# Optimization experiments

Hardware: AMD Instinct MI355X
Metric: run time of the kernel (lower is better)

The kernel has to match this reference:

```python
import jax, jax.numpy as jnp
import numpy as np

RNN = 64

def linear(x, W, b):
    return x @ W.T + b

def sample_logprob(key, logits):
    # Categorical(softmax(logits)): sample + log_prob of the sample
    s = jax.random.categorical(key, logits)
    lp = jnp.take_along_axis(jax.nn.log_softmax(logits, -1), s[:, None], 1)[:, 0]
    return s, lp

def lstm_encode(inst, embed, W_ih, W_hh, b_ih, b_hh):
    # torch.nn.LSTMCell unrolled over the sequence; gate order i,f,g,o
    x = embed[inst]                              # [B,S,64]
    B = inst.shape[0]
    def step(carry, xt):
        h, c = carry
        gates = xt @ W_ih.T + b_ih + h @ W_hh.T + b_hh   # [B,256]
        i, f, g, o = jnp.split(gates, 4, axis=-1)
        c = jax.nn.sigmoid(f) * c + jax.nn.sigmoid(i) * jnp.tanh(g)
        h = jax.nn.sigmoid(o) * jnp.tanh(c)
        return (h, c), None
    h0 = jnp.zeros((B, RNN), x.dtype)
    (h, _), _ = jax.lax.scan(step, (h0, h0), jnp.swapaxes(x, 0, 1))
    return h

def setup_inputs():
    key = jax.random.key(0)
    ks = jax.random.split(key, 20)
    B, S, V = 16384, 32, 1000
    def nrm(k, shape, scale=0.05):
        return jax.random.normal(k, shape, jnp.float32) * scale
    return {
        "inst0": jax.random.randint(ks[0], (B, S), 0, V + 1),
        "inst1": jax.random.randint(ks[1], (B, S), 0, V + 1),
        "canvas0": jax.random.randint(ks[2], (B, 25, 4), 0, 5).astype(jnp.int32),
        "canvas1": jax.random.randint(ks[3], (B, 25, 4), 0, 5).astype(jnp.int32),
        "ref": jax.random.randint(ks[4], (B, 4), 0, 5).astype(jnp.int32),
        "embed": nrm(ks[5], (V + 1, RNN)),
        "W_ih": nrm(ks[6], (4 * RNN, RNN)), "W_hh": nrm(ks[7], (4 * RNN, RNN)),
        "b_ih": jnp.zeros(4 * RNN), "b_hh": jnp.zeros(4 * RNN),
        "Wc": nrm(ks[8], (3, RNN)), "bc": jnp.zeros(3),
        "Ws": nrm(ks[9], (3, RNN)), "bs": jnp.zeros(3),
        "Wl": nrm(ks[10], (25, RNN)), "bl": jnp.zeros(25),
        "Wr1": nrm(ks[11], (32, RNN + 4)), "br1": jnp.zeros(32),
        "Wr2": nrm(ks[12], (1, 32)), "br2": jnp.zeros(1),
        "Wp": nrm(ks[13], (8, RNN)), "bp": jnp.zeros(8),
    }

def reference(inst0, inst1, canvas0, canvas1, ref, embed, W_ih, W_hh, b_ih, b_hh,
              Wc, bc, Ws, bs, Wl, bl, Wr1, br1, Wr2, br2, Wp, bp):
    B = inst0.shape[0]
    kk = jax.random.split(jax.random.key(42), 7)
    final_canvas = canvas1                                   # [B,25,4]

    def step_rewards(loc_predict, color_sample, shape_sample):
        valid = (loc_predict >= 0) & (loc_predict < 25)
        pt = jnp.take_along_axis(final_canvas,
                                 jnp.clip(loc_predict, 0, 24)[:, None, None],
                                 axis=1)[:, 0]               # [B,4]
        ok = valid & (pt.sum(-1) >= 0)
        loc_r = jnp.where(ok, 1.0, -1.0)
        col_r = jnp.where(ok, jnp.where(color_sample == pt[:, 0], 1.0, -1.0), 0.0)
        shp_r = jnp.where(ok, jnp.where(shape_sample == pt[:, 1], 1.0, -1.0), 0.0)
        return loc_r, col_r, shp_r

    # ---- dialog step 0: absolute location ----
    h0 = lstm_encode(inst0, embed, W_ih, W_hh, b_ih, b_hh)
    cs0, clp0 = sample_logprob(kk[0], linear(h0, Wc, bc))
    ss0, slp0 = sample_logprob(kk[1], linear(h0, Ws, bs))
    loc0, llp0 = sample_logprob(kk[2], linear(h0, Wl, bl))
    loc_r0, col_r0, _ = step_rewards(loc0, cs0, ss0)

    # ---- dialog step 1: relative location w.r.t. attended ref object ----
    h1 = lstm_encode(inst1, embed, W_ih, W_hh, b_ih, b_hh)
    cs1, clp1 = sample_logprob(kk[3], linear(h1, Wc, bc))
    ss1, slp1 = sample_logprob(kk[4], linear(h1, Ws, bs))
    ls1, llp1 = sample_logprob(kk[5], linear(h1, Wp, bp))    # 8-way offset
    prev = canvas0.astype(h1.dtype)                          # [B,25,4]
    feat = jnp.concatenate([jnp.broadcast_to(h1[:, None, :], (B, 25, RNN)), prev], 2)  # [B,25,68]
    att_logits = (jax.nn.relu(feat @ Wr1.T + br1) @ Wr2.T + br2)[:, :, 0]              # [B,25]
    att_sample, alp1 = sample_logprob(kk[6], att_logits)
    ref_obj = jnp.take_along_axis(canvas0, att_sample[:, None, None], axis=1)[:, 0]    # [B,4]
    att_reward = ((ref_obj == ref).sum(-1) == 4).astype(jnp.float32) * 2.0 - 1.0
    offsets = jnp.array([[-1, 0], [1, 0], [0, 1], [0, -1],
                         [-1, -1], [-1, 1], [1, -1], [1, 1]], jnp.int32)
    off = offsets[ls1]
    loc1 = (ref_obj[:, 2] + off[:, 0]) * 5 + (ref_obj[:, 3] + off[:, 1])
    loc_r1, col_r1, _ = step_rewards(loc1, cs1, ss1)

    logp = jnp.stack([clp0, slp0, llp0, clp1, slp1, llp1, alp1])          # [7,B]
    # NB: original appends step_loc_reward into shape_rewards (kept verbatim)
    rew = jnp.stack([loc_r0, col_r0, loc_r0, loc_r1, col_r1, loc_r1, att_reward])  # [7,B]
    return logp, rew
```

## Files before the change

kernel.cpp:

```cpp
#include <hip/hip_runtime.h>
#include <hip/hip_bf16.h>
#include <stdint.h>
#include <math.h>

#define NB 16384
#define NSEQ 32
#define NV 1001
#define NROWS 32768

#define CHK 272
#define RTG (8 * CHK)
#define SPL (2 * RTG)
#define HBUF (3 * SPL)

typedef __attribute__((ext_vector_type(8))) short bf16x8;
typedef __attribute__((ext_vector_type(4))) float f32x4;

__device__ __forceinline__ void tf2x32(uint32_t k0, uint32_t k1,
                                       uint32_t x0, uint32_t x1,
                                       uint32_t& o0, uint32_t& o1) {
  const uint32_t ks0 = k0, ks1 = k1, ks2 = k0 ^ k1 ^ 0x1BD11BDAu;
  x0 += ks0; x1 += ks1;
  const int rA[4] = {13, 15, 26, 6};
  const int rB[4] = {17, 29, 16, 24};
#pragma unroll
  for (int i = 0; i < 4; ++i) { x0 += x1; x1 = (x1 << rA[i]) | (x1 >> (32 - rA[i])); x1 ^= x0; }
  x0 += ks1; x1 += ks2 + 1u;
#pragma unroll
  for (int i = 0; i < 4; ++i) { x0 += x1; x1 = (x1 << rB[i]) | (x1 >> (32 - rB[i])); x1 ^= x0; }
  x0 += ks2; x1 += ks0 + 2u;
#pragma unroll
  for (int i = 0; i < 4; ++i) { x0 += x1; x1 = (x1 << rA[i]) | (x1 >> (32 - rA[i])); x1 ^= x0; }
  x0 += ks0; x1 += ks1 + 3u;
#pragma unroll
  for (int i = 0; i < 4; ++i) { x0 += x1; x1 = (x1 << rB[i]) | (x1 >> (32 - rB[i])); x1 ^= x0; }
  x0 += ks1; x1 += ks2 + 4u;
#pragma unroll
  for (int i = 0; i < 4; ++i) { x0 += x1; x1 = (x1 << rA[i]) | (x1 >> (32 - rA[i])); x1 ^= x0; }
  o0 = x0 + ks2; o1 = x1 + ks0 + 5u;
}

__device__ __forceinline__ float gumbel_from_bits(uint32_t bits) {
  uint32_t fb = (bits >> 9) | 0x3f800000u;
  float u = __uint_as_float(fb) - 1.0f;
  u = fmaxf(u, 1.17549435e-38f);
  return -logf(-logf(u));
}

__device__ __forceinline__ float sigm(float x) { return 1.0f / (1.0f + __expf(-x)); }
__device__ __forceinline__ float tanh_(float x) {
  float e = __expf(2.0f * x);
  return 1.0f - 2.0f / (e + 1.0f);
}

__device__ __forceinline__ float dot64(const float* __restrict__ w, const float* h) {
  float a = 0.f;
#pragma unroll
  for (int k = 0; k < 64; ++k) a = fmaf(w[k], h[k], a);
  return a;
}

__device__ __forceinline__ unsigned short bfbits(float x, float& xf) {
  __hip_bfloat16 hb = __float2bfloat16(x);
  xf = __bfloat162float(hb);
  unsigned short u;
  __builtin_memcpy(&u, &hb, 2);
  return u;
}

__device__ __forceinline__ uint32_t pkbf(float a, float b) {
  __hip_bfloat162 p = __float22bfloat162_rn(make_float2(a, b));
  uint32_t u; __builtin_memcpy(&u, &p, 4);
  return u;
}
__device__ __forceinline__ float lo16f(uint32_t w) { return __uint_as_float(w << 16); }
__device__ __forceinline__ float hi16f(uint32_t w) { return __uint_as_float(w & 0xffff0000u); }

__device__ __forceinline__ float lcell(const f32x4 A, const float4 es, float& c) {
  const float gi = A.x + es.x;
  const float gf = A.y + es.y;
  const float gg = A.z + es.z;
  const float go = A.w + es.w;
  const float ci = sigm(gf) * c + sigm(gi) * tanh_(gg);
  c = ci;
  return sigm(go) * tanh_(ci);
}

template <int N>
__device__ __forceinline__ void samp_team(const float* lg, int g, int C,
                                          uint32_t k0, uint32_t k1, int b,
                                          int& sOut, float& lpOut) {
  float m = -__builtin_inff();
#pragma unroll
  for (int i = 0; i < N; ++i) m = fmaxf(m, lg[i]);
  m = fmaxf(m, __shfl_xor(m, 1));
  m = fmaxf(m, __shfl_xor(m, 2));
  float se = 0.f;
#pragma unroll
  for (int i = 0; i < N; ++i) se += expf(lg[i] - m);
  se += __shfl_xor(se, 1);
  se += __shfl_xor(se, 2);
  const float lse = logf(se);
  float bz = -__builtin_inff(), bl = 0.f;
  int bi = 0x7fffffff;
#pragma unroll
  for (int i = 0; i < N; ++i) {
    const int c = g + 4 * i;
    uint32_t o0, o1; tf2x32(k0, k1, 0u, (uint32_t)(b * C + c), o0, o1);
    const float z = lg[i] + gumbel_from_bits(o0 ^ o1);
    if (z > bz || (z == bz && c < bi)) { bz = z; bi = c; bl = lg[i]; }
  }
#pragma unroll
  for (int d = 1; d <= 2; d <<= 1) {
    const float z2 = __shfl_xor(bz, d);
    const int i2 = __shfl_xor(bi, d);
    const float l2 = __shfl_xor(bl, d);
    if (z2 > bz || (z2 == bz && i2 < bi)) { bz = z2; bi = i2; bl = l2; }
  }
  sOut = bi;
  lpOut = (bl - m) - lse;
}

__global__ __launch_bounds__(256) void k_prep(
    const float* __restrict__ embed, const float* __restrict__ W_ih,
    const float* __restrict__ W_hh, const float* __restrict__ b_ih,
    const float* __restrict__ b_hh, float* __restrict__ embedWi,
    unsigned short* __restrict__ Wsp) {
  if (blockIdx.x >= NV) {
    int idx = (blockIdx.x - NV) * 256 + threadIdx.x;
    int s = idx >> 14;
    int rem = idx & 16383;
    int jp = rem >> 6, m = rem & 63;
    int kc = m >> 5, q = (m >> 3) & 3, p = m & 7;
    int k = kc * 32 + q * 8 + ((p >> 1) + ((p & 1) << 2));
    int j = (jp & 3) * 64 + (jp >> 2);
    float w = W_hh[j * 64 + k];
    float f1, f2, f3;
    unsigned short b1 = bfbits(w, f1);
    unsigned short b2 = bfbits(w - f1, f2);
    unsigned short b3 = bfbits(w - f1 - f2, f3);
    Wsp[idx] = (s == 0) ? b1 : (s == 1) ? b2 : b3;
    return;
  }
  __shared__ float er[64];
  int v = blockIdx.x;
  if (threadIdx.x < 64) er[threadIdx.x] = embed[v * 64 + threadIdx.x];
  __syncthreads();
  int jp = threadIdx.x;
  int j = (jp & 3) * 64 + (jp >> 2);
  float a = b_ih[j] + b_hh[j];
#pragma unroll
  for (int k = 0; k < 64; ++k) a = fmaf(W_ih[j * 64 + k], er[k], a);
  embedWi[v * 256 + jp] = a;
}

__global__ __launch_bounds__(512, 4) void k_lstm(
    const int* __restrict__ inst0, const int* __restrict__ inst1,
    const float* __restrict__ embedWi, const unsigned short* __restrict__ Wsp,
    float* __restrict__ hT) {
  extern __shared__ char smc[];
  int* idst = (int*)(smc + 2 * HBUF);

  const int tid = threadIdx.x;
  const int lane = tid & 63;
  const int e8 = tid >> 6;
  const int n15 = lane & 15;
  const int quad = lane >> 4;
  const int blk = blockIdx.x;
  const int rowbase = blk * 32;
  const int rb = (blk & 511) * 32;
  const int* __restrict__ inst = (blk < 512) ? inst0 : inst1;

  bf16x8 afr[2][2][3];
#pragma unroll
  for (int jt = 0; jt < 2; ++jt) {
    const int jrow = (e8 * 2 + jt) * 16 + n15;
#pragma unroll
    for (int kc = 0; kc < 2; ++kc)
#pragma unroll
      for (int s = 0; s < 3; ++s)
        afr[jt][kc][s] =
            *(const bf16x8*)(Wsp + ((s * 256 + jrow) * 64 + kc * 32 + quad * 8));
  }

  for (int i = tid; i < HBUF / 4; i += 512) ((float*)smc)[i] = 0.f;

  for (int i = tid; i < 1024; i += 512) {
    const int row = i >> 5, tt = i & 31;
    idst[tt * 32 + row] = inst[rb * NSEQ + i];
  }

  float cst[4];
#pragma unroll
  for (int i = 0; i < 4; ++i) cst[i] = 0.f;

  __syncthreads();

#pragma unroll 1
  for (int t = 0; t < NSEQ; ++t) {
    const char* __restrict__ hbr = smc + (t & 1) * HBUF;
    char* __restrict__ hbw = smc + ((t & 1) ^ 1) * HBUF;

    const int v0 = idst[t * 32 + n15];
    const int vn = idst[t * 32 + 16 + n15];
    float4 esc[2], esn[2];
#pragma unroll
    for (int jt = 0; jt < 2; ++jt) {
      esc[jt] = *(const float4*)(embedWi + v0 * 256 + (e8 * 8 + jt * 4 + quad) * 4);
      esn[jt] = *(const float4*)(embedWi + vn * 256 + (e8 * 8 + jt * 4 + quad) * 4);
    }

    bf16x8 b0[2][3], b1[2][3];
#pragma unroll
    for (int kc = 0; kc < 2; ++kc)
#pragma unroll
      for (int s = 0; s < 3; ++s) {
        b0[kc][s] = *(const bf16x8*)(hbr + s * SPL + 0 * RTG +
                                     (kc * 4 + quad) * CHK + n15 * 16);
        b1[kc][s] = *(const bf16x8*)(hbr + s * SPL + 1 * RTG +
                                     (kc * 4 + quad) * CHK + n15 * 16);
      }

    f32x4 a00 = (f32x4){0.f, 0.f, 0.f, 0.f};
#pragma unroll
    for (int kc = 0; kc < 2; ++kc) {
      a00 = __builtin_amdgcn_mfma_f32_16x16x32_bf16(afr[0][kc][0], b0[kc][2], a00, 0, 0, 0);
      a00 = __builtin_amdgcn_mfma_f32_16x16x32_bf16(afr[0][kc][2], b0[kc][0], a00, 0, 0, 0);
      a00 = __builtin_amdgcn_mfma_f32_16x16x32_bf16(afr[0][kc][1], b0[kc][1], a00, 0, 0, 0);
      a00 = __builtin_amdgcn_mfma_f32_16x16x32_bf16(afr[0][kc][0], b0[kc][1], a00, 0, 0, 0);
      a00 = __builtin_amdgcn_mfma_f32_16x16x32_bf16(afr[0][kc][1], b0[kc][0], a00, 0, 0, 0);
      a00 = __builtin_amdgcn_mfma_f32_16x16x32_bf16(afr[0][kc][0], b0[kc][0], a00, 0, 0, 0);
    }

    f32x4 a01 = (f32x4){0.f, 0.f, 0.f, 0.f};
#pragma unroll
    for (int kc = 0; kc < 2; ++kc) {
      a01 = __builtin_amdgcn_mfma_f32_16x16x32_bf16(afr[1][kc][0], b0[kc][2], a01, 0, 0, 0);
      a01 = __builtin_amdgcn_mfma_f32_16x16x32_bf16(afr[1][kc][2], b0[kc][0], a01, 0, 0, 0);
      a01 = __builtin_amdgcn_mfma_f32_16x16x32_bf16(afr[1][kc][1], b0[kc][1], a01, 0, 0, 0);
      a01 = __builtin_amdgcn_mfma_f32_16x16x32_bf16(afr[1][kc][0], b0[kc][1], a01, 0, 0, 0);
      a01 = __builtin_amdgcn_mfma_f32_16x16x32_bf16(afr[1][kc][1], b0[kc][0], a01, 0, 0, 0);
      a01 = __builtin_amdgcn_mfma_f32_16x16x32_bf16(afr[1][kc][0], b0[kc][0], a01, 0, 0, 0);
    }
    const float hv00 = lcell(a00, esc[0], cst[0]);

    f32x4 a10 = (f32x4){0.f, 0.f, 0.f, 0.f};
#pragma unroll
    for (int kc = 0; kc < 2; ++kc) {
      a10 = __builtin_amdgcn_mfma_f32_16x16x32_bf16(afr[0][kc][0], b1[kc][2], a10, 0, 0, 0);
      a10 = __builtin_amdgcn_mfma_f32_16x16x32_bf16(afr[0][kc][2], b1[kc][0], a10, 0, 0, 0);
      a10 = __builtin_amdgcn_mfma_f32_16x16x32_bf16(afr[0][kc][1], b1[kc][1], a10, 0, 0, 0);
      a10 = __builtin_amdgcn_mfma_f32_16x16x32_bf16(afr[0][kc][0], b1[kc][1], a10, 0, 0, 0);
      a10 = __builtin_amdgcn_mfma_f32_16x16x32_bf16(afr[0][kc][1], b1[kc][0], a10, 0, 0, 0);
      a10 = __builtin_amdgcn_mfma_f32_16x16x32_bf16(afr[0][kc][0], b1[kc][0], a10, 0, 0, 0);
    }
    const float hv10 = lcell(a01, esc[1], cst[2]);
    {
      const uint32_t w1 = pkbf(hv00, hv10);
      float d0 = hv00 - lo16f(w1), d1 = hv10 - hi16f(w1);
      const uint32_t w2 = pkbf(d0, d1);
      d0 -= lo16f(w2); d1 -= hi16f(w2);
      const uint32_t w3 = pkbf(d0, d1);
      char* base = hbw + 0 * RTG + e8 * CHK + n15 * 16 + quad * 4;
      *(uint32_t*)(base + 0 * SPL) = w1;
      *(uint32_t*)(base + 1 * SPL) = w2;
      *(uint32_t*)(base + 2 * SPL) = w3;
    }

    f32x4 a11 = (f32x4){0.f, 0.f, 0.f, 0.f};
#pragma unroll
    for (int kc = 0; kc < 2; ++kc) {
      a11 = __builtin_amdgcn_mfma_f32_16x16x32_bf16(afr[1][kc][0], b1[kc][2], a11, 0, 0, 0);
      a11 = __builtin_amdgcn_mfma_f32_16x16x32_bf16(afr[1][kc][2], b1[kc][0], a11, 0, 0, 0);
      a11 = __builtin_amdgcn_mfma_f32_16x16x32_bf16(afr[1][kc][1], b1[kc][1], a11, 0, 0, 0);
      a11 = __builtin_amdgcn_mfma_f32_16x16x32_bf16(afr[1][kc][0], b1[kc][1], a11, 0, 0, 0);
      a11 = __builtin_amdgcn_mfma_f32_16x16x32_bf16(afr[1][kc][1], b1[kc][0], a11, 0, 0, 0);
      a11 = __builtin_amdgcn_mfma_f32_16x16x32_bf16(afr[1][kc][0], b1[kc][0], a11, 0, 0, 0);
    }
    const float hv01 = lcell(a10, esn[0], cst[1]);

    const float hv11 = lcell(a11, esn[1], cst[3]);
    {
      const uint32_t w1 = pkbf(hv01, hv11);
      float d0 = hv01 - lo16f(w1), d1 = hv11 - hi16f(w1);
      const uint32_t w2 = pkbf(d0, d1);
      d0 -= lo16f(w2); d1 -= hi16f(w2);
      const uint32_t w3 = pkbf(d0, d1);
      char* base = hbw + 1 * RTG + e8 * CHK + n15 * 16 + quad * 4;
      *(uint32_t*)(base + 0 * SPL) = w1;
      *(uint32_t*)(base + 1 * SPL) = w2;
      *(uint32_t*)(base + 2 * SPL) = w3;
    }

    __builtin_amdgcn_sched_group_barrier(0x100, 14, 0);
    __builtin_amdgcn_sched_group_barrier(0x020, 4, 0);
#pragma unroll
    for (int i = 0; i < 12; ++i) {
      __builtin_amdgcn_sched_group_barrier(0x008, 1, 0);
      __builtin_amdgcn_sched_group_barrier(0x100, 1, 0);
    }
#pragma unroll
    for (int i = 0; i < 36; ++i) {
      __builtin_amdgcn_sched_group_barrier(0x008, 1, 0);
      __builtin_amdgcn_sched_group_barrier(0x002, 4, 0);
    }
    __builtin_amdgcn_sched_group_barrier(0x200, 6, 0);

    __syncthreads();
  }

#pragma unroll
  for (int rt = 0; rt < 2; ++rt) {
    const char* base = smc + rt * RTG + e8 * CHK + n15 * 16 + quad * 4;
    const uint32_t w1 = *(const uint32_t*)(base + 0 * SPL);
    const uint32_t w2 = *(const uint32_t*)(base + 1 * SPL);
    const uint32_t w3 = *(const uint32_t*)(base + 2 * SPL);
    const float hv0 = lo16f(w1) + lo16f(w2) + lo16f(w3);
    const float hv1 = hi16f(w1) + hi16f(w2) + hi16f(w3);
    hT[(e8 * 8 + 0 * 4 + quad) * NROWS + rowbase + rt * 16 + n15] = hv0;
    hT[(e8 * 8 + 1 * 4 + quad) * NROWS + rowbase + rt * 16 + n15] = hv1;
  }
}

__global__ __launch_bounds__(256) void k_heads(
    const int* __restrict__ canvas0, const int* __restrict__ canvas1,
    const int* __restrict__ ref,
    const float* __restrict__ Wc, const float* __restrict__ bc,
    const float* __restrict__ Ws, const float* __restrict__ bs,
    const float* __restrict__ Wl, const float* __restrict__ bl,
    const float* __restrict__ Wr1, const float* __restrict__ br1,
    const float* __restrict__ Wr2, const float* __restrict__ br2,
    const float* __restrict__ Wp, const float* __restrict__ bp,
    const float* __restrict__ hT, float* __restrict__ out) {
  const int tid = threadIdx.x;
  const int g = tid & 3;
  const int s = blockIdx.x & 1;
  const int b = (blockIdx.x >> 1) * 64 + (tid >> 2);
  const float NEG = -__builtin_inff();

  uint32_t kk0[7], kk1[7];
#pragma unroll
  for (int i = 0; i < 7; ++i) {
    uint32_t o0, o1; tf2x32(0u, 42u, 0u, (uint32_t)i, o0, o1);
    kk0[i] = o0; kk1[i] = o1;
  }

  float h[64];
#pragma unroll
  for (int u = 0; u < 64; ++u) h[u] = hT[u * NROWS + s * NB + b];

  float lgc[1], lgs[1];
  lgc[0] = (g < 3) ? (bc[g] + dot64(Wc + g * 64, h)) : NEG;
  lgs[0] = (g < 3) ? (bs[g] + dot64(Ws + g * 64, h)) : NEG;

  if (s == 0) {
    int cs0, ss0, loc0; float clp0, slp0, llp0;
    samp_team<1>(lgc, g, 3, kk0[0], kk1[0], b, cs0, clp0);
    samp_team<1>(lgs, g, 3, kk0[1], kk1[1], b, ss0, slp0);
    float lgl[7];
#pragma unroll
    for (int i = 0; i < 7; ++i) {
      const int cc = g + 4 * i;
      lgl[i] = (cc < 25) ? (bl[cc] + dot64(Wl + cc * 64, h)) : NEG;
    }
    samp_team<7>(lgl, g, 25, kk0[2], kk1[2], b, loc0, llp0);

    if (g == 0) {
      const int p0 = min(max(loc0, 0), 24);
      const int4 pt = ((const int4*)(canvas1 + b * 100))[p0];
      const bool ok0 = (loc0 >= 0) && (loc0 < 25) && (pt.x + pt.y + pt.z + pt.w >= 0);
      const float loc_r0 = ok0 ? 1.f : -1.f;
      const float col_r0 = ok0 ? ((cs0 == pt.x) ? 1.f : -1.f) : 0.f;
      out[0 * NB + b] = clp0;
      out[1 * NB + b] = slp0;
      out[2 * NB + b] = llp0;
      out[7 * NB + b] = loc_r0;
      out[8 * NB + b] = col_r0;
      out[9 * NB + b] = loc_r0;
    }
  } else {
    int cs1, ss1, ls1; float clp1, slp1, llp1;
    samp_team<1>(lgc, g, 3, kk0[3], kk1[3], b, cs1, clp1);
    samp_team<1>(lgs, g, 3, kk0[4], kk1[4], b, ss1, slp1);
    float lgp[2];
#pragma unroll
    for (int i = 0; i < 2; ++i) {
      const int cc = g + 4 * i;
      lgp[i] = bp[cc] + dot64(Wp + cc * 64, h);
    }
    samp_team<2>(lgp, g, 8, kk0[5], kk1[5], b, ls1, llp1);

    float uv8[8], w64[8], w65[8], w66[8], w67[8], wr2[8];
#pragma unroll
    for (int i = 0; i < 8; ++i) {
      const int j = g + 4 * i;
      uv8[i] = br1[j] + dot64(Wr1 + j * 68, h);
      const float* wr = Wr1 + j * 68 + 64;
      w64[i] = wr[0]; w65[i] = wr[1]; w66[i] = wr[2]; w67[i] = wr[3];
      wr2[i] = Wr2[j];
    }
    float lgA[7];
#pragma unroll
    for (int i = 0; i < 7; ++i) lgA[i] = NEG;
    const float b2 = br2[0];
#pragma unroll
    for (int p = 0; p < 25; ++p) {
      const int4 c4 = ((const int4*)(canvas0 + b * 100))[p];
      const float f0 = (float)c4.x, f1 = (float)c4.y;
      const float f2 = (float)c4.z, f3 = (float)c4.w;
      float part = 0.f;
#pragma unroll
      for (int i = 0; i < 8; ++i) {
        float hj = uv8[i];
        hj = fmaf(w64[i], f0, hj);
        hj = fmaf(w65[i], f1, hj);
        hj = fmaf(w66[i], f2, hj);
        hj = fmaf(w67[i], f3, hj);
        part = fmaf(wr2[i], fmaxf(hj, 0.f), part);
      }
      part += __shfl_xor(part, 1);
      part += __shfl_xor(part, 2);
      const float ap = b2 + part;
      if ((p & 3) == g) lgA[p >> 2] = ap;
    }
    int att_s; float alp1;
    samp_team<7>(lgA, g, 25, kk0[6], kk1[6], b, att_s, alp1);

    if (g == 0) {
      const int4 r4 = ((const int4*)(canvas0 + b * 100))[att_s];
      const int4 rr = *(const int4*)(ref + b * 4);
      const bool match = (r4.x == rr.x) && (r4.y == rr.y) &&
                         (r4.z == rr.z) && (r4.w == rr.w);
      const float att_reward = match ? 1.f : -1.f;
      const int ox = (int)((0x22001120u >> (ls1 * 4)) & 0xFu) - 1;
      const int oy = (int)((0x20200211u >> (ls1 * 4)) & 0xFu) - 1;
      const int loc1 = (r4.z + ox) * 5 + (r4.w + oy);
      const int p1 = min(max(loc1, 0), 24);
      const int4 q4 = ((const int4*)(canvas1 + b * 100))[p1];
      const bool ok1 = (loc1 >= 0) && (loc1 < 25) && (q4.x + q4.y + q4.z + q4.w >= 0);
      const float loc_r1 = ok1 ? 1.f : -1.f;
      const float col_r1 = ok1 ? ((cs1 == q4.x) ? 1.f : -1.f) : 0.f;
      out[3 * NB + b]  = clp1;
      out[4 * NB + b]  = slp1;
      out[5 * NB + b]  = llp1;
      out[6 * NB + b]  = alp1;
      out[10 * NB + b] = loc_r1;
      out[11 * NB + b] = col_r1;
      out[12 * NB + b] = loc_r1;
      out[13 * NB + b] = att_reward;
    }
  }
}

extern "C" void kernel_launch(void* const* d_in, const int* in_sizes, int n_in,
                              void* d_out, int out_size, void* d_ws, size_t ws_size,
                              hipStream_t stream) {
  const int* inst0 = (const int*)d_in[0];
  const int* inst1 = (const int*)d_in[1];
  const int* canvas0 = (const int*)d_in[2];
  const int* canvas1 = (const int*)d_in[3];
  const int* ref = (const int*)d_in[4];
  const float* embed = (const float*)d_in[5];
  const float* W_ih = (const float*)d_in[6];
  const float* W_hh = (const float*)d_in[7];
  const float* b_ih = (const float*)d_in[8];
  const float* b_hh = (const float*)d_in[9];
  const float* Wc = (const float*)d_in[10];
  const float* bc = (const float*)d_in[11];
  const float* Ws = (const float*)d_in[12];
  const float* bs = (const float*)d_in[13];
  const float* Wl = (const float*)d_in[14];
  const float* bl = (const float*)d_in[15];
  const float* Wr1 = (const float*)d_in[16];
  const float* br1 = (const float*)d_in[17];
  const float* Wr2 = (const float*)d_in[18];
  const float* br2 = (const float*)d_in[19];
  const float* Wp = (const float*)d_in[20];
  const float* bp = (const float*)d_in[21];

  float* ws = (float*)d_ws;
  float* embedWi = ws;
  unsigned short* Wsp = (unsigned short*)(ws + NV * 256);
  float* hT = ws + NV * 256 + 24576;
  float* out = (float*)d_out;

  const size_t ldsBytes = 2 * HBUF + 4096;
  k_prep<<<NV + 192, 256, 0, stream>>>(embed, W_ih, W_hh, b_ih, b_hh, embedWi, Wsp);
  k_lstm<<<1024, 512, ldsBytes, stream>>>(inst0, inst1, embedWi, Wsp, hT);
  k_heads<<<512, 256, 0, stream>>>(canvas0, canvas1, ref, Wc, bc, Ws, bs,
                                   Wl, bl, Wr1, br1, Wr2, br2, Wp, bp, hT, out);
}
```

Measured before the change: 423.3 us.

## Fuse head sampling into LSTM kernel via LDS hidden-state handoff

Merges the separate heads kernel into the LSTM kernel: the final hidden state of each block's 32 rows is staged in padded LDS, and 128 threads then compute the head logits, sampling and rewards directly. This drops one kernel launch and the global round trip of the transposed hidden-state buffer. It also removes the explicit sched_group_barrier instruction-scheduling hints from the recurrent loop, leaving scheduling to the compiler. The cost is more LDS per block, which may reduce occupancy, and a serial tail in which most threads sit idle while the heads run.

```diff
diff --git a/kernel.cpp b/kernel.cpp
--- a/kernel.cpp
+++ b/kernel.cpp
@@ -12,6 +12,8 @@
 #define RTG (8 * CHK)
 #define SPL (2 * RTG)
 #define HBUF (3 * SPL)
+#define IDSOFF (2 * HBUF)
+#define HLOFF (2 * HBUF + 4096)
 
 typedef __attribute__((ext_vector_type(8))) short bf16x8;
 typedef __attribute__((ext_vector_type(4))) float f32x4;
@@ -157,9 +159,18 @@
 __global__ __launch_bounds__(512, 4) void k_lstm(
     const int* __restrict__ inst0, const int* __restrict__ inst1,
     const float* __restrict__ embedWi, const unsigned short* __restrict__ Wsp,
-    float* __restrict__ hT) {
+    const int* __restrict__ canvas0, const int* __restrict__ canvas1,
+    const int* __restrict__ ref,
+    const float* __restrict__ Wc, const float* __restrict__ bc,
+    const float* __restrict__ Ws, const float* __restrict__ bs,
+    const float* __restrict__ Wl, const float* __restrict__ bl,
+    const float* __restrict__ Wr1, const float* __restrict__ br1,
+    const float* __restrict__ Wr2, const float* __restrict__ br2,
+    const float* __restrict__ Wp, const float* __restrict__ bp,
+    float* __restrict__ out) {
   extern __shared__ char smc[];
-  int* idst = (int*)(smc + 2 * HBUF);
+  int* idst = (int*)(smc + IDSOFF);
+  float* hL = (float*)(smc + HLOFF);
 
   const int tid = threadIdx.x;
   const int lane = tid & 63;
@@ -167,7 +178,6 @@
   const int n15 = lane & 15;
   const int quad = lane >> 4;
   const int blk = blockIdx.x;
-  const int rowbase = blk * 32;
   const int rb = (blk & 511) * 32;
   const int* __restrict__ inst = (blk < 512) ? inst0 : inst1;
 
@@ -292,20 +302,6 @@
       *(uint32_t*)(base + 2 * SPL) = w3;
     }
 
-    __builtin_amdgcn_sched_group_barrier(0x100, 14, 0);
-    __builtin_amdgcn_sched_group_barrier(0x020, 4, 0);
-#pragma unroll
-    for (int i = 0; i < 12; ++i) {
-      __builtin_amdgcn_sched_group_barrier(0x008, 1, 0);
-      __builtin_amdgcn_sched_group_barrier(0x100, 1, 0);
-    }
-#pragma unroll
-    for (int i = 0; i < 36; ++i) {
-      __builtin_amdgcn_sched_group_barrier(0x008, 1, 0);
-      __builtin_amdgcn_sched_group_barrier(0x002, 4, 0);
-    }
-    __builtin_amdgcn_sched_group_barrier(0x200, 6, 0);
-
     __syncthreads();
   }
 
@@ -317,25 +313,16 @@
     const uint32_t w3 = *(const uint32_t*)(base + 2 * SPL);
     const float hv0 = lo16f(w1) + lo16f(w2) + lo16f(w3);
     const float hv1 = hi16f(w1) + hi16f(w2) + hi16f(w3);
-    hT[(e8 * 8 + 0 * 4 + quad) * NROWS + rowbase + rt * 16 + n15] = hv0;
-    hT[(e8 * 8 + 1 * 4 + quad) * NROWS + rowbase + rt * 16 + n15] = hv1;
-  }
-}
-
-__global__ __launch_bounds__(256) void k_heads(
-    const int* __restrict__ canvas0, const int* __restrict__ canvas1,
-    const int* __restrict__ ref,
-    const float* __restrict__ Wc, const float* __restrict__ bc,
-    const float* __restrict__ Ws, const float* __restrict__ bs,
-    const float* __restrict__ Wl, const float* __restrict__ bl,
-    const float* __restrict__ Wr1, const float* __restrict__ br1,
-    const float* __restrict__ Wr2, const float* __restrict__ br2,
-    const float* __restrict__ Wp, const float* __restrict__ bp,
-    const float* __restrict__ hT, float* __restrict__ out) {
-  const int tid = threadIdx.x;
+    const int row = rt * 16 + n15;
+    hL[row * 65 + e8 * 8 + 0 + quad] = hv0;
+    hL[row * 65 + e8 * 8 + 4 + quad] = hv1;
+  }
+  __syncthreads();
+
+  if (tid >= 128) return;
   const int g = tid & 3;
-  const int s = blockIdx.x & 1;
-  const int b = (blockIdx.x >> 1) * 64 + (tid >> 2);
+  const int r = tid >> 2;
+  const int b = rb + r;
   const float NEG = -__builtin_inff();
 
   uint32_t kk0[7], kk1[7];
@@ -347,13 +334,13 @@
 
   float h[64];
 #pragma unroll
-  for (int u = 0; u < 64; ++u) h[u] = hT[u * NROWS + s * NB + b];
+  for (int u = 0; u < 64; ++u) h[u] = hL[r * 65 + u];
 
   float lgc[1], lgs[1];
   lgc[0] = (g < 3) ? (bc[g] + dot64(Wc + g * 64, h)) : NEG;
   lgs[0] = (g < 3) ? (bs[g] + dot64(Ws + g * 64, h)) : NEG;
 
-  if (s == 0) {
+  if (blk < 512) {
     int cs0, ss0, loc0; float clp0, slp0, llp0;
     samp_team<1>(lgc, g, 3, kk0[0], kk1[0], b, cs0, clp0);
     samp_team<1>(lgs, g, 3, kk0[1], kk1[1], b, ss0, slp0);
@@ -481,12 +468,12 @@
   float* ws = (float*)d_ws;
   float* embedWi = ws;
   unsigned short* Wsp = (unsigned short*)(ws + NV * 256);
-  float* hT = ws + NV * 256 + 24576;
   float* out = (float*)d_out;
 
-  const size_t ldsBytes = 2 * HBUF + 4096;
+  const size_t ldsBytes = HLOFF + 32 * 65 * 4;
   k_prep<<<NV + 192, 256, 0, stream>>>(embed, W_ih, W_hh, b_ih, b_hh, embedWi, Wsp);
-  k_lstm<<<1024, 512, ldsBytes, stream>>>(inst0, inst1, embedWi, Wsp, hT);
-  k_heads<<<512, 256, 0, stream>>>(canvas0, canvas1, ref, Wc, bc, Ws, bs,
-                                   Wl, bl, Wr1, br1, Wr2, br2, Wp, bp, hT, out);
-}
+  k_lstm<<<1024, 512, ldsBytes, stream>>>(inst0, inst1, embedWi, Wsp,
+                                          canvas0, canvas1, ref,
+                                          Wc, bc, Ws, bs, Wl, bl,
+                                          Wr1, br1, Wr2, br2, Wp, bp, out);
+}
```

Result: slower. 489.9 us (+15.7%).
